# Kernel optimization log

Hardware: AMD Instinct MI355X
Metric: run time of the kernel (lower is better)

## Reference

```python
import jax, jax.numpy as jnp
import numpy as np

HEAD_DIM = 64
N_HEADS = 16
D_MODEL = 2048
SEQ = 2048
BATCH = 1
LAYER_IDX = 12
LN_EPS = 1e-5


def setup_inputs() -> dict:
    key = jax.random.key(0)
    ks = jax.random.split(key, 8)
    s = 0.02
    return {
        "x": jax.random.normal(ks[0], (BATCH, SEQ, D_MODEL), dtype=jnp.float32),
        "W_qkv": jax.random.normal(ks[1], (3 * N_HEADS * 2 * HEAD_DIM, D_MODEL), dtype=jnp.float32) * s,
        "W_o": jax.random.normal(ks[2], (D_MODEL, D_MODEL), dtype=jnp.float32) * s,
        "lambda_q1": jax.random.normal(ks[3], (2 * HEAD_DIM,), dtype=jnp.float32) * 0.1,
        "lambda_k1": jax.random.normal(ks[4], (2 * HEAD_DIM,), dtype=jnp.float32) * 0.1,
        "lambda_q2": jax.random.normal(ks[5], (2 * HEAD_DIM,), dtype=jnp.float32) * 0.1,
        "lambda_k2": jax.random.normal(ks[6], (2 * HEAD_DIM,), dtype=jnp.float32) * 0.1,
        "gn_gamma": jnp.ones((N_HEADS, 2 * HEAD_DIM), dtype=jnp.float32),
        "gn_beta": jnp.zeros((N_HEADS, 2 * HEAD_DIM), dtype=jnp.float32),
    }


def _causal_sdpa(q, k, v, scale):
    # q,k: [B,H,S,d], v: [B,H,S,2d]
    S = q.shape[2]
    scores = jnp.einsum("bhqd,bhkd->bhqk", q, k) * scale
    causal = jnp.tril(jnp.ones((S, S), dtype=bool))
    scores = jnp.where(causal[None, None], scores, jnp.float32(-1e30))
    attn = jax.nn.softmax(scores, axis=-1)
    return jnp.einsum("bhqk,bhkd->bhqd", attn, v)


def reference(x, W_qkv, W_o, lambda_q1, lambda_k1, lambda_q2, lambda_k2, gn_gamma, gn_beta):
    B, S, D = x.shape
    lambda_init = 0.8 - 0.6 * jnp.exp(jnp.float32(-0.3 * LAYER_IDX))
    scale = HEAD_DIM ** -0.5

    qkv = x @ W_qkv.T  # [B,S,6*H*d]
    qkv = qkv.reshape(B, S, 3, N_HEADS, 2 * HEAD_DIM)
    q = jnp.transpose(qkv[:, :, 0], (0, 2, 1, 3))  # [B,H,S,2d]
    k = jnp.transpose(qkv[:, :, 1], (0, 2, 1, 3))
    v = jnp.transpose(qkv[:, :, 2], (0, 2, 1, 3))
    q1, q2 = q[..., :HEAD_DIM], q[..., HEAD_DIM:]
    k1, k2 = k[..., :HEAD_DIM], k[..., HEAD_DIM:]

    lam = jnp.exp(lambda_q1 * lambda_k1) - jnp.exp(lambda_q2 * lambda_k2) + lambda_init  # [2d]

    A1 = _causal_sdpa(q1, k1, v, scale)
    A2 = _causal_sdpa(q2, k2, v, scale)
    out = A1 - lam * A2  # broadcast over value channel [B,H,S,2d]

    # per-head LayerNorm over last dim
    mu = jnp.mean(out, axis=-1, keepdims=True)
    var = jnp.mean((out - mu) ** 2, axis=-1, keepdims=True)
    out = (out - mu) * jax.lax.rsqrt(var + LN_EPS)
    out = out * gn_gamma[None, :, None, :] + gn_beta[None, :, None, :]

    out = out * (1.0 - lambda_init)
    out = jnp.transpose(out, (0, 2, 1, 3)).reshape(B, S, D)
    return out @ W_o.T
```

## Files before the change

kernel.cpp:

```cpp
#include <hip/hip_runtime.h>

typedef short short8 __attribute__((ext_vector_type(8)));
typedef float f32x4 __attribute__((ext_vector_type(4)));
typedef unsigned short u16;
typedef u16 u16x8 __attribute__((ext_vector_type(8)));
typedef u16 u16x4 __attribute__((ext_vector_type(4)));

__device__ static inline u16 f2bf(float f) {
    union { float f; unsigned u; } v; v.f = f;
    unsigned r = v.u + 0x7fffu + ((v.u >> 16) & 1u);
    return (u16)(r >> 16);
}

__device__ static inline unsigned cvt_pk_bf16(float a, float b) {
    unsigned r;
    asm("v_cvt_pk_bf16_f32 %0, %1, %2" : "=v"(r) : "v"(a), "v"(b));
    return r;
}

__global__ __launch_bounds__(256) void cast_kernel(const float* __restrict__ in,
                                                   u16* __restrict__ out, int n) {
    int i = (blockIdx.x * 256 + threadIdx.x) * 4;
    if (i + 3 < n) {
        f32x4 v = *(const f32x4*)&in[i];
        u16x4 o;
        o[0] = f2bf(v[0]); o[1] = f2bf(v[1]); o[2] = f2bf(v[2]); o[3] = f2bf(v[3]);
        *(u16x4*)&out[i] = o;
    }
}

template <int BM, int BN, int MODE, int MINW>
__global__ __launch_bounds__(256, MINW) void gemm_bt(const u16* __restrict__ A,
                                                     const u16* __restrict__ B,
                                                     int M, int N, int K,
                                                     float* __restrict__ C,
                                                     u16* __restrict__ Qo,
                                                     u16* __restrict__ Ko,
                                                     u16* __restrict__ Vo) {
    constexpr int APT = BM * 4 / 256;
    constexpr int BPT = BN * 4 / 256;
    constexpr int MT = BM / 32, NT = BN / 32;
    __shared__ u16 As[BM * 32];
    __shared__ u16 Bs[BN * 32];
    const int tid  = threadIdx.x;
    const int lane = tid & 63, wave = tid >> 6;
    const int quad = lane >> 4, l15 = lane & 15;
    const int wm = wave >> 1, wn = wave & 1;
    const int m0 = blockIdx.y * BM;
    const int n0 = blockIdx.x * BN;

    f32x4 acc[MT][NT] = {};

    const u16* aga[APT];
    const u16* bga[BPT];
#pragma unroll
    for (int i = 0; i < APT; i++) {
        int s = tid + i * 256, r = s >> 2;
        int kg = (s & 3) ^ ((r >> 1) & 3);
        aga[i] = &A[(size_t)(m0 + r) * K + kg * 8];
    }
#pragma unroll
    for (int i = 0; i < BPT; i++) {
        int s = tid + i * 256, r = s >> 2;
        int kg = (s & 3) ^ ((r >> 1) & 3);
        bga[i] = &B[(size_t)(n0 + r) * K + kg * 8];
    }

    u16x8 ast[APT], bst[BPT];
#pragma unroll
    for (int i = 0; i < APT; i++) ast[i] = *(const u16x8*)aga[i];
#pragma unroll
    for (int i = 0; i < BPT; i++) bst[i] = *(const u16x8*)bga[i];

    for (int k0 = 0; k0 < K; k0 += 32) {
        if (k0) __syncthreads();
#pragma unroll
        for (int i = 0; i < APT; i++) *(u16x8*)&As[(tid + i * 256) * 8] = ast[i];
#pragma unroll
        for (int i = 0; i < BPT; i++) *(u16x8*)&Bs[(tid + i * 256) * 8] = bst[i];
        __syncthreads();
        if (k0 + 32 < K) {
#pragma unroll
            for (int i = 0; i < APT; i++) ast[i] = *(const u16x8*)(aga[i] + k0 + 32);
#pragma unroll
            for (int i = 0; i < BPT; i++) bst[i] = *(const u16x8*)(bga[i] + k0 + 32);
        }

        short8 af[MT], bf[NT];
#pragma unroll
        for (int mt = 0; mt < MT; mt++) {
            int row = wm * (BM / 2) + mt * 16 + l15;
            int slot = row * 4 + (quad ^ ((row >> 1) & 3));
            af[mt] = *(const short8*)&As[slot * 8];
        }
#pragma unroll
        for (int nt = 0; nt < NT; nt++) {
            int row = wn * (BN / 2) + nt * 16 + l15;
            int slot = row * 4 + (quad ^ ((row >> 1) & 3));
            bf[nt] = *(const short8*)&Bs[slot * 8];
        }
#pragma unroll
        for (int mt = 0; mt < MT; mt++)
#pragma unroll
            for (int nt = 0; nt < NT; nt++)
                acc[mt][nt] = __builtin_amdgcn_mfma_f32_16x16x32_bf16(af[mt], bf[nt], acc[mt][nt], 0, 0, 0);
    }

    if (MODE == 0) {
#pragma unroll
        for (int mt = 0; mt < MT; mt++)
#pragma unroll
            for (int nt = 0; nt < NT; nt++)
#pragma unroll
                for (int r = 0; r < 4; r++) {
                    int row = m0 + wm * (BM / 2) + mt * 16 + quad * 4 + r;
                    int col = n0 + wn * (BN / 2) + nt * 16 + l15;
                    C[(size_t)row * N + col] = acc[mt][nt][r];
                }
    } else {
        const int comp = n0 >> 11, h = (n0 >> 7) & 15;
        u16* dst = (comp == 0) ? Qo : ((comp == 1) ? Ko : Vo);
        const float sc = (comp == 0) ? 0.18033688f : 1.0f;
#pragma unroll
        for (int mt = 0; mt < MT; mt++)
#pragma unroll
            for (int nt = 0; nt < NT; nt++)
#pragma unroll
                for (int r = 0; r < 4; r++) {
                    int row = m0 + wm * (BM / 2) + mt * 16 + quad * 4 + r;
                    int d = wn * (BN / 2) + nt * 16 + l15;
                    dst[((h * 2048) + row) * 128 + d] = f2bf(acc[mt][nt][r] * sc);
                }
    }
}

__global__ __launch_bounds__(256) void transpose_v(const u16* __restrict__ vb,
                                                   u16* __restrict__ vT) {
    __shared__ u16 T[64 * 136];
    const int s0 = blockIdx.x * 64, h = blockIdx.y;
    const int tid = threadIdx.x;
#pragma unroll
    for (int i = 0; i < 4; i++) {
        int c = tid + i * 256;
        int s = c >> 4, dch = c & 15;
        *(u16x8*)&T[s * 136 + dch * 8] =
            *(const u16x8*)&vb[((h * 2048) + s0 + s) * 128 + dch * 8];
    }
    __syncthreads();
#pragma unroll
    for (int i = 0; i < 4; i++) {
        int c = tid + i * 256;
        int d = c >> 3, sch = c & 7;
        u16x8 o;
#pragma unroll
        for (int j = 0; j < 8; j++) o[j] = T[(sch * 8 + j) * 136 + d];
        *(u16x8*)&vT[((h * 128) + d) * 2048 + s0 + sch * 8] = o;
    }
}

__global__ __launch_bounds__(256, 2) void attn_kernel(const u16* __restrict__ qb,
                                                      const u16* __restrict__ kb,
                                                      const u16* __restrict__ vT,
                                                      float* __restrict__ ob) {
    const int bid = blockIdx.x;
    const int h = bid & 15;
    const int comp = (bid >> 4) & 1;
    const int j = bid >> 5;
    const int J = (j < 8) ? (2 * j + 1) : (30 - 2 * j);
    const int nkt = 2 * J + 2;
    const int q0 = J * 128;
    const int tid = threadIdx.x, lane = tid & 63, wave = tid >> 6;
    const int quad = lane >> 4, l15 = lane & 15;
    const int qh = quad >> 1, ql = quad & 1;

    __shared__ u16 Ks[64 * 64];
    __shared__ u16 VsT[128 * 64];
    const char* KsB = (const char*)Ks;
    const char* VsB = (const char*)VsT;

    const u16* kb_h = &kb[(size_t)h * 2048 * 128 + comp * 64];
    const u16* vT_h = &vT[(size_t)h * 128 * 2048];

    const int c1 = tid, c2 = tid + 256;
    const int k1key = c1 >> 3, k1dc = ((c1 & 7) ^ k1key) & 7;
    const int k2key = c2 >> 3, k2dc = ((c2 & 7) ^ k2key) & 7;
    const u16* kaddr1 = &kb_h[k1key * 128 + k1dc * 8];
    const u16* kaddr2 = &kb_h[k2key * 128 + k2dc * 8];
    const u16* vaddr[4];
#pragma unroll
    for (int i = 0; i < 4; i++) {
        int c = tid + i * 256;
        int dim = c >> 3, kc = ((c & 7) ^ dim) & 7;
        vaddr[i] = &vT_h[dim * 2048 + kc * 8];
    }

    const int koff0 = l15 * 128 + ((quad ^ l15) & 7) * 16;
    const int koff1 = l15 * 128 + (((quad + 4) ^ l15) & 7) * 16;
    int vb[8][2];
#pragma unroll
    for (int nt = 0; nt < 8; nt++) {
        int dim = nt * 16 + l15;
        int base = dim * 128 + ((qh ^ dim) & 7) * 16 + ql * 8;
        vb[nt][0] = base;
        vb[nt][1] = base ^ 64;
    }

    short8 aq[2][2];
#pragma unroll
    for (int qs = 0; qs < 2; qs++)
#pragma unroll
        for (int ks = 0; ks < 2; ks++) {
            int qrow = q0 + wave * 32 + qs * 16 + l15;
            aq[qs][ks] = *(const short8*)
                &qb[((h * 2048) + qrow) * 128 + comp * 64 + ks * 32 + quad * 8];
        }

    float l_acc[2] = {0.f, 0.f};
    f32x4 acc[8][2] = {};

    u16x8 kst0, kst1, vst[4];
    kst0 = *(const u16x8*)kaddr1;
    kst1 = *(const u16x8*)kaddr2;
#pragma unroll
    for (int i = 0; i < 4; i++) vst[i] = *(const u16x8*)vaddr[i];
    const u16* kp1 = kaddr1 + 8192;
    const u16* kp2 = kaddr2 + 8192;
    const u16* vp[4];
#pragma unroll
    for (int i = 0; i < 4; i++) vp[i] = vaddr[i] + 64;

    for (int kt = 0; kt < nkt; kt++) {
        *(u16x8*)&Ks[c1 * 8] = kst0;
        *(u16x8*)&Ks[c2 * 8] = kst1;
#pragma unroll
        for (int i = 0; i < 4; i++) *(u16x8*)&VsT[(tid + i * 256) * 8] = vst[i];
        __syncthreads();

        if (kt + 1 < nkt) {
            kst0 = *(const u16x8*)kp1; kp1 += 8192;
            kst1 = *(const u16x8*)kp2; kp2 += 8192;
#pragma unroll
            for (int i = 0; i < 4; i++) { vst[i] = *(const u16x8*)vp[i]; vp[i] += 64; }
        }

        short8 kf[4][2];
#pragma unroll
        for (int kn = 0; kn < 4; kn++) {
            kf[kn][0] = *(const short8*)(KsB + (koff0 + kn * 2048));
            kf[kn][1] = *(const short8*)(KsB + (koff1 + kn * 2048));
        }

        short8 b8[2][2];
#pragma unroll
        for (int qs = 0; qs < 2; qs++) {
#pragma unroll
            for (int kn2 = 0; kn2 < 2; kn2++) {
                f32x4 sa = {}, sb = {};
                sa = __builtin_amdgcn_mfma_f32_16x16x32_bf16(kf[2 * kn2][0], aq[qs][0], sa, 0, 0, 0);
                sa = __builtin_amdgcn_mfma_f32_16x16x32_bf16(kf[2 * kn2][1], aq[qs][1], sa, 0, 0, 0);
                sb = __builtin_amdgcn_mfma_f32_16x16x32_bf16(kf[2 * kn2 + 1][0], aq[qs][0], sb, 0, 0, 0);
                sb = __builtin_amdgcn_mfma_f32_16x16x32_bf16(kf[2 * kn2 + 1][1], aq[qs][1], sb, 0, 0, 0);
                if (kt >= nkt - 2) {
                    int q = q0 + wave * 32 + qs * 16 + l15;
                    int kb0 = kt * 64 + kn2 * 32 + quad * 4;
#pragma unroll
                    for (int r = 0; r < 4; r++) {
                        if (kb0 + r > q) sa[r] = -1e30f;
                        if (kb0 + 16 + r > q) sb[r] = -1e30f;
                    }
                }
                float p0 = exp2f(sa[0]), p1 = exp2f(sa[1]), p2 = exp2f(sa[2]), p3 = exp2f(sa[3]);
                float p4 = exp2f(sb[0]), p5 = exp2f(sb[1]), p6 = exp2f(sb[2]), p7 = exp2f(sb[3]);
                l_acc[qs] += ((p0 + p1) + (p2 + p3)) + ((p4 + p5) + (p6 + p7));
                union { unsigned w[4]; short8 s; } pw;
                pw.w[0] = cvt_pk_bf16(p0, p1);
                pw.w[1] = cvt_pk_bf16(p2, p3);
                pw.w[2] = cvt_pk_bf16(p4, p5);
                pw.w[3] = cvt_pk_bf16(p6, p7);
                b8[qs][kn2] = pw.s;
            }
        }

        __builtin_amdgcn_s_setprio(1);
#pragma unroll
        for (int nt = 0; nt < 8; nt++) {
#pragma unroll
            for (int kn2 = 0; kn2 < 2; kn2++) {
                union { u16x4 h4[2]; short8 s; } av;
                int o0 = vb[nt][kn2];
                av.h4[0] = *(const u16x4*)(VsB + o0);
                av.h4[1] = *(const u16x4*)(VsB + (o0 ^ 32));
                acc[nt][0] = __builtin_amdgcn_mfma_f32_16x16x32_bf16(av.s, b8[0][kn2], acc[nt][0], 0, 0, 0);
                acc[nt][1] = __builtin_amdgcn_mfma_f32_16x16x32_bf16(av.s, b8[1][kn2], acc[nt][1], 0, 0, 0);
            }
        }
        __builtin_amdgcn_s_setprio(0);
        __syncthreads();
    }

#pragma unroll
    for (int qs = 0; qs < 2; qs++) {
        l_acc[qs] += __shfl_xor(l_acc[qs], 16);
        l_acc[qs] += __shfl_xor(l_acc[qs], 32);
    }
    float rl[2] = {1.f / l_acc[0], 1.f / l_acc[1]};

#pragma unroll
    for (int qs = 0; qs < 2; qs++) {
        int s = q0 + wave * 32 + qs * 16 + l15;
        float* orow = &ob[((size_t)(comp * 16 + h) * 2048 + s) * 128 + quad * 4];
#pragma unroll
        for (int nt = 0; nt < 8; nt++) {
            f32x4 v;
#pragma unroll
            for (int r = 0; r < 4; r++) v[r] = acc[nt][qs][r] * rl[qs];
            *(f32x4*)&orow[nt * 16] = v;
        }
    }
}

__global__ __launch_bounds__(256) void combine_kernel(const float* __restrict__ ob,
                                                      const float* __restrict__ lq1,
                                                      const float* __restrict__ lk1,
                                                      const float* __restrict__ lq2,
                                                      const float* __restrict__ lk2,
                                                      const float* __restrict__ gamma,
                                                      const float* __restrict__ beta,
                                                      u16* __restrict__ attn) {
    const int tid = threadIdx.x, wave = tid >> 6, lane = tid & 63;
    const int row = blockIdx.x * 4 + wave;
    const int s = row >> 4, h = row & 15;
    const float lambda_init = 0.8f - 0.6f * __expf(-3.6f);
    const int d0 = lane * 2;
    float vals[2];
#pragma unroll
    for (int j = 0; j < 2; j++) {
        int d = d0 + j;
        float a1 = ob[((h)*2048 + s) * 128 + d];
        float a2 = ob[((16 + h) * 2048 + s) * 128 + d];
        float lam = __expf(lq1[d] * lk1[d]) - __expf(lq2[d] * lk2[d]) + lambda_init;
        vals[j] = a1 - lam * a2;
    }
    float sum = vals[0] + vals[1];
    float sq = vals[0] * vals[0] + vals[1] * vals[1];
#pragma unroll
    for (int off = 1; off < 64; off <<= 1) {
        sum += __shfl_xor(sum, off);
        sq += __shfl_xor(sq, off);
    }
    float mu = sum * (1.f / 128.f);
    float var = sq * (1.f / 128.f) - mu * mu;
    float rinv = rsqrtf(var + 1e-5f);
    float osc = 1.f - lambda_init;
#pragma unroll
    for (int j = 0; j < 2; j++) {
        int d = d0 + j;
        float g = gamma[h * 128 + d], b = beta[h * 128 + d];
        float v = ((vals[j] - mu) * rinv * g + b) * osc;
        attn[s * 2048 + h * 128 + d] = f2bf(v);
    }
}

extern "C" void kernel_launch(void* const* d_in, const int* in_sizes, int n_in,
                              void* d_out, int out_size, void* d_ws, size_t ws_size,
                              hipStream_t stream) {
    (void)in_sizes; (void)n_in; (void)out_size; (void)ws_size;
    const float* x    = (const float*)d_in[0];
    const float* Wqkv = (const float*)d_in[1];
    const float* Wo   = (const float*)d_in[2];
    const float* lq1  = (const float*)d_in[3];
    const float* lk1  = (const float*)d_in[4];
    const float* lq2  = (const float*)d_in[5];
    const float* lk2  = (const float*)d_in[6];
    const float* gam  = (const float*)d_in[7];
    const float* bet  = (const float*)d_in[8];
    float* out = (float*)d_out;

    char* ws = (char*)d_ws;
    u16*   xb    = (u16*)(ws);
    u16*   wqkvb = (u16*)(ws + (size_t)(8 << 20));
    float* ob    = (float*)(ws + (size_t)(8 << 20));
    u16*   wob   = (u16*)(ws + (size_t)(40 << 20));
    u16*   qb    = (u16*)(ws + (size_t)(48 << 20));
    u16*   kb    = (u16*)(ws + (size_t)(56 << 20));
    u16*   vb    = (u16*)(ws + (size_t)(64 << 20));
    u16*   vT    = (u16*)(ws + (size_t)(72 << 20));
    u16*   attn  = (u16*)(ws);

    cast_kernel<<<(2048 * 2048) / 1024, 256, 0, stream>>>(x, xb, 2048 * 2048);
    cast_kernel<<<(6144 * 2048) / 1024, 256, 0, stream>>>(Wqkv, wqkvb, 6144 * 2048);
    cast_kernel<<<(2048 * 2048) / 1024, 256, 0, stream>>>(Wo, wob, 2048 * 2048);
    gemm_bt<128, 128, 1, 3><<<dim3(48, 16), 256, 0, stream>>>(
        xb, wqkvb, 2048, 6144, 2048, nullptr, qb, kb, vb);
    transpose_v<<<dim3(32, 16), 256, 0, stream>>>(vb, vT);
    attn_kernel<<<512, 256, 0, stream>>>(qb, kb, vT, ob);
    combine_kernel<<<8192, 256, 0, stream>>>(ob, lq1, lk1, lq2, lk2, gam, bet, attn);
    gemm_bt<128, 64, 0, 2><<<dim3(32, 16), 256, 0, stream>>>(
        attn, wob, 2048, 2048, 2048, out, nullptr, nullptr, nullptr);
}
```

Measured before the change: 286.7 us.

## Fuse fp32-to-bf16 casts into GEMM tile loads, drop separate cast kernels

Removes the three standalone cast kernels for x, W_qkv and W_o. The GEMM instead loads fp32 tiles directly and converts them to bf16 with packed conversion instructions before writing to shared memory. This saves the extra launches and the write-then-reread of bf16 copies. In exchange each GEMM tile load reads twice as many bytes from global memory, uses more registers for staging, and rounds with the hardware convert instead of the software f2bf.

New measurement: 320.0 us. +11.6%, slower.

```diff
diff --git a/kernel.cpp b/kernel.cpp
--- a/kernel.cpp
+++ b/kernel.cpp
@@ -18,20 +18,18 @@
     return r;
 }
 
-__global__ __launch_bounds__(256) void cast_kernel(const float* __restrict__ in,
-                                                   u16* __restrict__ out, int n) {
-    int i = (blockIdx.x * 256 + threadIdx.x) * 4;
-    if (i + 3 < n) {
-        f32x4 v = *(const f32x4*)&in[i];
-        u16x4 o;
-        o[0] = f2bf(v[0]); o[1] = f2bf(v[1]); o[2] = f2bf(v[2]); o[3] = f2bf(v[3]);
-        *(u16x4*)&out[i] = o;
-    }
-}
-
-template <int BM, int BN, int MODE, int MINW>
-__global__ __launch_bounds__(256, MINW) void gemm_bt(const u16* __restrict__ A,
-                                                     const u16* __restrict__ B,
+__device__ static inline u16x8 pack_bf8(const f32x4& lo, const f32x4& hi) {
+    union { unsigned w[4]; u16x8 s; } u;
+    u.w[0] = cvt_pk_bf16(lo[0], lo[1]);
+    u.w[1] = cvt_pk_bf16(lo[2], lo[3]);
+    u.w[2] = cvt_pk_bf16(hi[0], hi[1]);
+    u.w[3] = cvt_pk_bf16(hi[2], hi[3]);
+    return u.s;
+}
+
+template <int BM, int BN, int MODE, int MINW, int AF, int BF>
+__global__ __launch_bounds__(256, MINW) void gemm_bt(const void* __restrict__ Av,
+                                                     const void* __restrict__ Bv,
                                                      int M, int N, int K,
                                                      float* __restrict__ C,
                                                      u16* __restrict__ Qo,
@@ -49,41 +47,68 @@
     const int m0 = blockIdx.y * BM;
     const int n0 = blockIdx.x * BN;
 
+    const u16*   A16 = (const u16*)Av;
+    const float* A32 = (const float*)Av;
+    const u16*   B16 = (const u16*)Bv;
+    const float* B32 = (const float*)Bv;
+
     f32x4 acc[MT][NT] = {};
 
-    const u16* aga[APT];
-    const u16* bga[BPT];
+    size_t aoff[APT], boff[BPT];
 #pragma unroll
     for (int i = 0; i < APT; i++) {
         int s = tid + i * 256, r = s >> 2;
         int kg = (s & 3) ^ ((r >> 1) & 3);
-        aga[i] = &A[(size_t)(m0 + r) * K + kg * 8];
+        aoff[i] = (size_t)(m0 + r) * K + kg * 8;
     }
 #pragma unroll
     for (int i = 0; i < BPT; i++) {
         int s = tid + i * 256, r = s >> 2;
         int kg = (s & 3) ^ ((r >> 1) & 3);
-        bga[i] = &B[(size_t)(n0 + r) * K + kg * 8];
-    }
-
-    u16x8 ast[APT], bst[BPT];
-#pragma unroll
-    for (int i = 0; i < APT; i++) ast[i] = *(const u16x8*)aga[i];
-#pragma unroll
-    for (int i = 0; i < BPT; i++) bst[i] = *(const u16x8*)bga[i];
+        boff[i] = (size_t)(n0 + r) * K + kg * 8;
+    }
+
+    u16x8 ast16[APT], bst16[BPT];
+    f32x4 astf[APT][2], bstf[BPT][2];
+#pragma unroll
+    for (int i = 0; i < APT; i++) {
+        if (AF) { astf[i][0] = *(const f32x4*)&A32[aoff[i]];
+                  astf[i][1] = *(const f32x4*)&A32[aoff[i] + 4]; }
+        else    { ast16[i] = *(const u16x8*)&A16[aoff[i]]; }
+    }
+#pragma unroll
+    for (int i = 0; i < BPT; i++) {
+        if (BF) { bstf[i][0] = *(const f32x4*)&B32[boff[i]];
+                  bstf[i][1] = *(const f32x4*)&B32[boff[i] + 4]; }
+        else    { bst16[i] = *(const u16x8*)&B16[boff[i]]; }
+    }
 
     for (int k0 = 0; k0 < K; k0 += 32) {
         if (k0) __syncthreads();
 #pragma unroll
-        for (int i = 0; i < APT; i++) *(u16x8*)&As[(tid + i * 256) * 8] = ast[i];
-#pragma unroll
-        for (int i = 0; i < BPT; i++) *(u16x8*)&Bs[(tid + i * 256) * 8] = bst[i];
+        for (int i = 0; i < APT; i++) {
+            u16x8 v = AF ? pack_bf8(astf[i][0], astf[i][1]) : ast16[i];
+            *(u16x8*)&As[(tid + i * 256) * 8] = v;
+        }
+#pragma unroll
+        for (int i = 0; i < BPT; i++) {
+            u16x8 v = BF ? pack_bf8(bstf[i][0], bstf[i][1]) : bst16[i];
+            *(u16x8*)&Bs[(tid + i * 256) * 8] = v;
+        }
         __syncthreads();
         if (k0 + 32 < K) {
 #pragma unroll
-            for (int i = 0; i < APT; i++) ast[i] = *(const u16x8*)(aga[i] + k0 + 32);
-#pragma unroll
-            for (int i = 0; i < BPT; i++) bst[i] = *(const u16x8*)(bga[i] + k0 + 32);
+            for (int i = 0; i < APT; i++) {
+                if (AF) { astf[i][0] = *(const f32x4*)&A32[aoff[i] + k0 + 32];
+                          astf[i][1] = *(const f32x4*)&A32[aoff[i] + k0 + 36]; }
+                else    { ast16[i] = *(const u16x8*)&A16[aoff[i] + k0 + 32]; }
+            }
+#pragma unroll
+            for (int i = 0; i < BPT; i++) {
+                if (BF) { bstf[i][0] = *(const f32x4*)&B32[boff[i] + k0 + 32];
+                          bstf[i][1] = *(const f32x4*)&B32[boff[i] + k0 + 36]; }
+                else    { bst16[i] = *(const u16x8*)&B16[boff[i] + k0 + 32]; }
+            }
         }
 
         short8 af[MT], bf[NT];
@@ -377,24 +402,18 @@
     float* out = (float*)d_out;
 
     char* ws = (char*)d_ws;
-    u16*   xb    = (u16*)(ws);
-    u16*   wqkvb = (u16*)(ws + (size_t)(8 << 20));
-    float* ob    = (float*)(ws + (size_t)(8 << 20));
-    u16*   wob   = (u16*)(ws + (size_t)(40 << 20));
-    u16*   qb    = (u16*)(ws + (size_t)(48 << 20));
-    u16*   kb    = (u16*)(ws + (size_t)(56 << 20));
-    u16*   vb    = (u16*)(ws + (size_t)(64 << 20));
-    u16*   vT    = (u16*)(ws + (size_t)(72 << 20));
-    u16*   attn  = (u16*)(ws);
-
-    cast_kernel<<<(2048 * 2048) / 1024, 256, 0, stream>>>(x, xb, 2048 * 2048);
-    cast_kernel<<<(6144 * 2048) / 1024, 256, 0, stream>>>(Wqkv, wqkvb, 6144 * 2048);
-    cast_kernel<<<(2048 * 2048) / 1024, 256, 0, stream>>>(Wo, wob, 2048 * 2048);
-    gemm_bt<128, 128, 1, 3><<<dim3(48, 16), 256, 0, stream>>>(
-        xb, wqkvb, 2048, 6144, 2048, nullptr, qb, kb, vb);
+    u16*   attn = (u16*)(ws);
+    float* ob   = (float*)(ws + (size_t)(8 << 20));
+    u16*   qb   = (u16*)(ws + (size_t)(48 << 20));
+    u16*   kb   = (u16*)(ws + (size_t)(56 << 20));
+    u16*   vb   = (u16*)(ws + (size_t)(64 << 20));
+    u16*   vT   = (u16*)(ws + (size_t)(72 << 20));
+
+    gemm_bt<128, 128, 1, 3, 1, 1><<<dim3(48, 16), 256, 0, stream>>>(
+        (const void*)x, (const void*)Wqkv, 2048, 6144, 2048, nullptr, qb, kb, vb);
     transpose_v<<<dim3(32, 16), 256, 0, stream>>>(vb, vT);
     attn_kernel<<<512, 256, 0, stream>>>(qb, kb, vT, ob);
     combine_kernel<<<8192, 256, 0, stream>>>(ob, lq1, lk1, lq2, lk2, gam, bet, attn);
-    gemm_bt<128, 64, 0, 2><<<dim3(32, 16), 256, 0, stream>>>(
-        attn, wob, 2048, 2048, 2048, out, nullptr, nullptr, nullptr);
-}
+    gemm_bt<128, 64, 0, 2, 0, 1><<<dim3(32, 16), 256, 0, stream>>>(
+        (const void*)attn, (const void*)Wo, 2048, 2048, 2048, out, nullptr, nullptr, nullptr);
+}
```
